# Optimization experiments

Hardware: AMD Instinct MI355X
Metric: run time of the kernel (lower is better)

The kernel has to match this reference:

```python
import jax, jax.numpy as jnp
import numpy as np

NUM_USERS = 1_000_000
NUM_ITEMS = 500_000
EMB = 64
H1, H2 = 256, 128
BATCH = 16384
BN_EPS = 1e-5


def setup_inputs() -> dict:
    key = jax.random.key(0)
    ks = jax.random.split(key, 16)
    inp = {
        "user_indices": jax.random.randint(ks[0], (BATCH,), 0, NUM_USERS),
        "item_indices": jax.random.randint(ks[1], (BATCH,), 0, NUM_ITEMS),
        # wide linear over concatenated one-hots == weight vector of len U+I
        "wide_w": jax.random.normal(ks[2], (NUM_USERS + NUM_ITEMS,), jnp.float32) * 0.01,
        "wide_b": jnp.zeros((1,), jnp.float32),
        "user_table": jax.random.normal(ks[3], (NUM_USERS, EMB), jnp.float32) * 0.05,
        "item_table": jax.random.normal(ks[4], (NUM_ITEMS, EMB), jnp.float32) * 0.05,
        "W1": jax.random.normal(ks[5], (H1, 2 * EMB), jnp.float32) * (1.0 / np.sqrt(2 * EMB)),
        "b1": jnp.zeros((H1,), jnp.float32),
        "g1": jnp.ones((H1,), jnp.float32),
        "be1": jnp.zeros((H1,), jnp.float32),
        "W2": jax.random.normal(ks[6], (H2, H1), jnp.float32) * (1.0 / np.sqrt(H1)),
        "b2": jnp.zeros((H2,), jnp.float32),
        "g2": jnp.ones((H2,), jnp.float32),
        "be2": jnp.zeros((H2,), jnp.float32),
        "W3": jax.random.normal(ks[7], (1, H2), jnp.float32) * (1.0 / np.sqrt(H2)),
        "b3": jnp.zeros((1,), jnp.float32),
    }
    return inp


def _block(x, W, b, g, be):
    # Linear -> ReLU -> BatchNorm1d (training-mode batch stats); Dropout is identity in eval.
    h = jnp.maximum(x @ W.T + b, 0.0)
    mu = jnp.mean(h, axis=0)
    var = jnp.mean((h - mu) ** 2, axis=0)  # biased var, as torch BN normalization
    return g * (h - mu) * jax.lax.rsqrt(var + BN_EPS) + be


def reference(user_indices, item_indices, wide_w, wide_b, user_table, item_table,
              W1, b1, g1, be1, W2, b2, g2, be2, W3, b3):
    # Wide path: one-hot scatter + Linear(.,1) == 2-row gather of wide_w + bias
    wide = wide_w[user_indices] + wide_w[item_indices + user_table.shape[0]] + wide_b[0]  # (B,)
    # Deep path
    x = jnp.concatenate([user_table[user_indices], item_table[item_indices]], axis=1)  # (B, 2E)
    h = _block(x, W1, b1, g1, be1)
    h = _block(h, W2, b2, g2, be2)
    deep = h @ W3.T + b3  # (B, 1)
    return jax.nn.sigmoid(wide[:, None] + deep)
```

## Files before the change

kernel.cpp:

```cpp
#include <hip/hip_runtime.h>
#include <math.h>

constexpr float INV_B = 1.0f / 16384.0f;
constexpr float BN_EPS_C = 1e-5f;
constexpr int NUM_USERS_C = 1000000;

typedef __attribute__((ext_vector_type(8))) short bf16x8;
typedef __attribute__((ext_vector_type(4))) float f32x4;

__device__ inline unsigned short f2bf(float f) {
    union { float f; unsigned u; } v; v.f = f;
    unsigned r = v.u + 0x7FFFu + ((v.u >> 16) & 1u);
    return (unsigned short)(r >> 16);
}
__device__ inline float bf2f(unsigned short h) {
    union { unsigned u; float f; } v; v.u = ((unsigned)h) << 16; return v.f;
}
__device__ inline bf16x8 pack8(float4 a, float4 b) {
    bf16x8 sv;
    sv[0] = (short)f2bf(a.x); sv[1] = (short)f2bf(a.y);
    sv[2] = (short)f2bf(a.z); sv[3] = (short)f2bf(a.w);
    sv[4] = (short)f2bf(b.x); sv[5] = (short)f2bf(b.y);
    sv[6] = (short)f2bf(b.z); sv[7] = (short)f2bf(b.w);
    return sv;
}
__device__ inline unsigned swz256(int r, int kb) { return (unsigned)(r * 256 + (kb ^ ((r & 7) << 4))); }
__device__ inline unsigned swz512(int r, int kb) { return (unsigned)(r * 512 + (kb ^ ((r & 7) << 4))); }

__global__ __launch_bounds__(256) void wd_k0(
    const float* __restrict__ W1, const float* __restrict__ W2,
    unsigned short* __restrict__ img1, unsigned short* __restrict__ img2,
    float* __restrict__ stats)
{
    int t = blockIdx.x * 256 + threadIdx.x;
    if (t < 12288) stats[t] = 0.f;
    if (t < 4096) {
        int a = t * 16, n = a >> 8, ks = a & 255;
        int k0 = (ks ^ ((n & 7) << 4)) >> 1;
        const float* src = W1 + (size_t)n * 128 + k0;
        float4 va = ((const float4*)src)[0];
        float4 vb = ((const float4*)src)[1];
        *(bf16x8*)((char*)img1 + a) = pack8(va, vb);
    } else if (t < 8192) {
        int tt = t - 4096;
        int a = tt * 16, h = a >> 15, rem = a & 32767, n = rem >> 8, ks = rem & 255;
        int kb = ks ^ ((n & 7) << 4);
        int k0 = h * 128 + (kb >> 1);
        const float* src = W2 + (size_t)n * 256 + k0;
        float4 va = ((const float4*)src)[0];
        float4 vb = ((const float4*)src)[1];
        *(bf16x8*)((char*)img2 + a) = pack8(va, vb);
    }
}

__global__ __launch_bounds__(512, 4) void wd_k1(
    const int* __restrict__ ui, const int* __restrict__ ii,
    const float* __restrict__ utab, const float* __restrict__ itab,
    const unsigned short* __restrict__ img1, const float* __restrict__ b1,
    unsigned short* __restrict__ h1s, float* __restrict__ part1)
{
    __shared__ char Xs[8192];
    __shared__ char Bnc[16384];
    __shared__ float sstat[512];

    const int tid = threadIdx.x, bid = blockIdx.x, row0 = bid * 32;
    const int w = tid >> 6, lane = tid & 63, lr = lane & 15, lk = lane >> 4;

    bf16x8 bfr[2][4];
#pragma unroll
    for (int nj = 0; nj < 2; ++nj) {
        int n = w * 32 + nj * 16 + lr;
        const char* bp = (const char*)img1 + n * 256;
        int sx = (n & 7) << 4;
#pragma unroll
        for (int kst = 0; kst < 4; ++kst)
            bfr[nj][kst] = *(const bf16x8*)(bp + ((kst * 64 + lk * 16) ^ sx));
    }

    {
        int row = tid >> 4, kc = tid & 15;
        const float* src = (kc < 8)
            ? utab + (size_t)ui[row0 + row] * 64 + kc * 8
            : itab + (size_t)ii[row0 + row] * 64 + (kc - 8) * 8;
        float4 a = ((const float4*)src)[0];
        float4 b = ((const float4*)src)[1];
        *(bf16x8*)(Xs + swz256(row, kc * 16)) = pack8(a, b);
    }
    __syncthreads();

    f32x4 acc[2][2];
#pragma unroll
    for (int mi = 0; mi < 2; ++mi)
#pragma unroll
        for (int nj = 0; nj < 2; ++nj) acc[mi][nj] = (f32x4){0.f, 0.f, 0.f, 0.f};

#pragma unroll
    for (int kst = 0; kst < 4; ++kst) {
        int kb = kst * 64 + lk * 16;
        bf16x8 a0 = *(const bf16x8*)(Xs + swz256(lr, kb));
        bf16x8 a1v = *(const bf16x8*)(Xs + swz256(16 + lr, kb));
#pragma unroll
        for (int nj = 0; nj < 2; ++nj) {
            acc[0][nj] = __builtin_amdgcn_mfma_f32_16x16x32_bf16(a0, bfr[nj][kst], acc[0][nj], 0, 0, 0);
            acc[1][nj] = __builtin_amdgcn_mfma_f32_16x16x32_bf16(a1v, bfr[nj][kst], acc[1][nj], 0, 0, 0);
        }
    }

#pragma unroll
    for (int nj = 0; nj < 2; ++nj) {
        int col = w * 32 + nj * 16 + lr;
        float bias = b1[col];
        float s = 0.f, q = 0.f;
#pragma unroll
        for (int mi = 0; mi < 2; ++mi)
#pragma unroll
            for (int reg = 0; reg < 4; ++reg) {
                int rl = mi * 16 + lk * 4 + reg;
                float v = fmaxf(acc[mi][nj][reg] + bias, 0.f);
                unsigned short hb = f2bf(v);
                float vr = bf2f(hb);
                s += vr; q += vr * vr;
                *(unsigned short*)(Bnc + swz512(rl, col * 2)) = hb;
            }
        s += __shfl_xor(s, 16); s += __shfl_xor(s, 32);
        q += __shfl_xor(q, 16); q += __shfl_xor(q, 32);
        if (lk == 0) { sstat[col] = s; sstat[256 + col] = q; }
    }
    __syncthreads();

    {
        const char* s0 = Bnc + tid * 32;
        char* d0 = (char*)h1s + (size_t)bid * 16384 + tid * 32;
        *(bf16x8*)d0 = *(const bf16x8*)s0;
        *(bf16x8*)(d0 + 16) = *(const bf16x8*)(s0 + 16);
    }
    atomicAdd(&part1[(size_t)(bid & 15) * 512 + tid], sstat[tid]);
}

__global__ __launch_bounds__(512, 4) void wd_k2(
    const unsigned short* __restrict__ h1s, const float* __restrict__ part1,
    const float* __restrict__ g1, const float* __restrict__ be1,
    const unsigned short* __restrict__ img2, const float* __restrict__ b2,
    unsigned short* __restrict__ h2s, float* __restrict__ part2)
{
    __shared__ char As[16384];
    __shared__ char Bnc[8192];
    __shared__ float a1s[256], c1s[256], sstat[256];

    const int tid = threadIdx.x, bid = blockIdx.x;
    const int w = tid >> 6, lane = tid & 63, lr = lane & 15, lk = lane >> 4;
    const int n = w * 16 + lr;
    const int sx = (n & 7) << 4;

    bf16x8 bfr[8];
#pragma unroll
    for (int h = 0; h < 2; ++h)
#pragma unroll
        for (int kst = 0; kst < 4; ++kst)
            bfr[h * 4 + kst] = *(const bf16x8*)((const char*)img2 + h * 32768 + n * 256 + ((kst * 64 + lk * 16) ^ sx));

    if (tid < 256) {
        float s = 0.f, q = 0.f;
#pragma unroll
        for (int r = 0; r < 16; ++r) { s += part1[r * 512 + tid]; q += part1[r * 512 + 256 + tid]; }
        float mu = s * INV_B;
        float var = fmaf(q, INV_B, -mu * mu);
        float rs = rsqrtf(var + BN_EPS_C);
        float a = g1[tid] * rs;
        a1s[tid] = a;
        c1s[tid] = fmaf(-mu, a, be1[tid]);
    }
    __syncthreads();

#pragma unroll
    for (int it = 0; it < 2; ++it) {
        int a = (it * 512 + tid) * 16;
        int r = a >> 9, ks = a & 511;
        int k0 = (ks ^ ((r & 7) << 4)) >> 1;
        bf16x8 hv = *(const bf16x8*)((const char*)h1s + (size_t)bid * 16384 + a);
        bf16x8 sv;
#pragma unroll
        for (int j = 0; j < 8; ++j) {
            float f = bf2f((unsigned short)hv[j]);
            f = fmaf(a1s[k0 + j], f, c1s[k0 + j]);
            sv[j] = (short)f2bf(f);
        }
        *(bf16x8*)(As + a) = sv;
    }
    __syncthreads();

    f32x4 acc[2];
    acc[0] = (f32x4){0.f, 0.f, 0.f, 0.f};
    acc[1] = (f32x4){0.f, 0.f, 0.f, 0.f};
#pragma unroll
    for (int k8 = 0; k8 < 8; ++k8) {
        int kb = (k8 * 64 + lk * 16) ^ ((lr & 7) << 4);
        bf16x8 a0 = *(const bf16x8*)(As + lr * 512 + kb);
        bf16x8 a1v = *(const bf16x8*)(As + (16 + lr) * 512 + kb);
        acc[0] = __builtin_amdgcn_mfma_f32_16x16x32_bf16(a0, bfr[k8], acc[0], 0, 0, 0);
        acc[1] = __builtin_amdgcn_mfma_f32_16x16x32_bf16(a1v, bfr[k8], acc[1], 0, 0, 0);
    }

    {
        float bias = b2[n];
        float s = 0.f, q = 0.f;
#pragma unroll
        for (int mi = 0; mi < 2; ++mi)
#pragma unroll
            for (int reg = 0; reg < 4; ++reg) {
                int rl = mi * 16 + lk * 4 + reg;
                float v = fmaxf(acc[mi][reg] + bias, 0.f);
                unsigned short hb = f2bf(v);
                float vr = bf2f(hb);
                s += vr; q += vr * vr;
                *(unsigned short*)(Bnc + swz256(rl, n * 2)) = hb;
            }
        s += __shfl_xor(s, 16); s += __shfl_xor(s, 32);
        q += __shfl_xor(q, 16); q += __shfl_xor(q, 32);
        if (lk == 0) { sstat[n] = s; sstat[128 + n] = q; }
    }
    __syncthreads();

    *(bf16x8*)((char*)h2s + (size_t)bid * 8192 + tid * 16) = *(const bf16x8*)(Bnc + tid * 16);
    if (tid < 256) atomicAdd(&part2[(size_t)(bid & 15) * 256 + tid], sstat[tid]);
}

__global__ __launch_bounds__(256, 2) void wd_k3(
    const int* __restrict__ ui, const int* __restrict__ ii,
    const float* __restrict__ wide_w, const float* __restrict__ wide_b,
    const unsigned short* __restrict__ h2s, const float* __restrict__ part2,
    const float* __restrict__ g2, const float* __restrict__ be2,
    const float* __restrict__ W3, const float* __restrict__ b3,
    float* __restrict__ out)
{
    __shared__ float af[128], cf[128];
    const int tid = threadIdx.x, bid = blockIdx.x;
    const int r = tid >> 2, kq = tid & 3;
    const int row = bid * 64 + r;

    float wide = 0.f;
    if (kq == 0) wide = wide_w[ui[row]] + wide_w[NUM_USERS_C + ii[row]];

    if (tid < 128) {
        float s = 0.f, q = 0.f;
#pragma unroll
        for (int rr = 0; rr < 16; ++rr) { s += part2[rr * 256 + tid]; q += part2[rr * 256 + 128 + tid]; }
        float mu = s * INV_B;
        float var = fmaf(q, INV_B, -mu * mu);
        float rs = rsqrtf(var + BN_EPS_C);
        float a = g2[tid] * rs;
        float c = fmaf(-mu, a, be2[tid]);
        float w3 = W3[tid];
        af[tid] = a * w3;
        cf[tid] = c * w3;
    }
    __syncthreads();

    const int tile = row >> 5, rin = row & 31;
    const char* tb = (const char*)h2s + (size_t)tile * 8192 + rin * 256;
    float acc = 0.f;
#pragma unroll
    for (int j = 0; j < 4; ++j) {
        int ks = (kq * 64 + j * 16) ^ ((rin & 7) << 4);
        bf16x8 hv = *(const bf16x8*)(tb + ks);
#pragma unroll
        for (int e = 0; e < 8; ++e) {
            float h = bf2f((unsigned short)hv[e]);
            int k = kq * 32 + j * 8 + e;
            acc += fmaf(h, af[k], cf[k]);
        }
    }
    acc += __shfl_xor(acc, 1);
    acc += __shfl_xor(acc, 2);
    if (kq == 0) {
        float logit = acc + b3[0] + wide_b[0] + wide;
        out[row] = 1.f / (1.f + expf(-logit));
    }
}

extern "C" void kernel_launch(void* const* d_in, const int* in_sizes, int n_in,
                              void* d_out, int out_size, void* d_ws, size_t ws_size,
                              hipStream_t stream)
{
    const int*   ui     = (const int*)d_in[0];
    const int*   ii     = (const int*)d_in[1];
    const float* wide_w = (const float*)d_in[2];
    const float* wide_b = (const float*)d_in[3];
    const float* utab   = (const float*)d_in[4];
    const float* itab   = (const float*)d_in[5];
    const float* W1     = (const float*)d_in[6];
    const float* b1     = (const float*)d_in[7];
    const float* g1     = (const float*)d_in[8];
    const float* be1    = (const float*)d_in[9];
    const float* W2     = (const float*)d_in[10];
    const float* b2     = (const float*)d_in[11];
    const float* g2     = (const float*)d_in[12];
    const float* be2    = (const float*)d_in[13];
    const float* W3     = (const float*)d_in[14];
    const float* b3     = (const float*)d_in[15];
    float* outp = (float*)d_out;

    char* base = (char*)d_ws;
    float* part1 = (float*)base;
    float* part2 = (float*)(base + 16 * 512 * 4);
    unsigned short* img1 = (unsigned short*)(base + 49152);
    unsigned short* img2 = (unsigned short*)(base + 49152 + 65536);
    unsigned short* h1s  = (unsigned short*)(base + 49152 + 131072);
    unsigned short* h2s  = (unsigned short*)(base + 49152 + 131072 + (size_t)512 * 16384);

    wd_k0<<<48, 256, 0, stream>>>(W1, W2, img1, img2, part1);
    wd_k1<<<512, 512, 0, stream>>>(ui, ii, utab, itab, img1, b1, h1s, part1);
    wd_k2<<<512, 512, 0, stream>>>(h1s, part1, g1, be1, img2, b2, h2s, part2);
    wd_k3<<<256, 256, 0, stream>>>(ui, ii, wide_w, wide_b, h2s, part2, g2, be2, W3, b3, outp);
}
```

Baseline: 28.99 us.

## Fuse all stages into one persistent kernel with grid barriers for BN stats

Replaces the four-kernel pipeline with a single 256-block kernel. Each block handles 64 rows end to end, keeping the hidden activations in shared memory, and uses global atomic counters as grid-wide barriers to wait for the batch-norm statistics. Weight repacking to bf16 now happens per block directly from fp32 in registers, removing the prep kernel. The layer-3 dot product is folded into the layer-2 epilogue through shuffles. This removes launch overhead and the global round trips for h1 and h2. The cost is redundant weight conversion in every block and a spin barrier that deadlocks unless all 256 blocks are co-resident.

After: 65.99 us. 128% more time.

```diff
diff --git a/kernel.cpp b/kernel.cpp
--- a/kernel.cpp
+++ b/kernel.cpp
@@ -4,6 +4,7 @@
 constexpr float INV_B = 1.0f / 16384.0f;
 constexpr float BN_EPS_C = 1e-5f;
 constexpr int NUM_USERS_C = 1000000;
+#define NBLK 256
 
 typedef __attribute__((ext_vector_type(8))) short bf16x8;
 typedef __attribute__((ext_vector_type(4))) float f32x4;
@@ -27,58 +28,51 @@
 __device__ inline unsigned swz256(int r, int kb) { return (unsigned)(r * 256 + (kb ^ ((r & 7) << 4))); }
 __device__ inline unsigned swz512(int r, int kb) { return (unsigned)(r * 512 + (kb ^ ((r & 7) << 4))); }
 
-__global__ __launch_bounds__(256) void wd_k0(
-    const float* __restrict__ W1, const float* __restrict__ W2,
-    unsigned short* __restrict__ img1, unsigned short* __restrict__ img2,
-    float* __restrict__ stats)
+__device__ inline void gbar(int* cnt) {
+    __syncthreads();
+    if (threadIdx.x == 0) {
+        __threadfence();
+        __hip_atomic_fetch_add(cnt, 1, __ATOMIC_ACQ_REL, __HIP_MEMORY_SCOPE_AGENT);
+        while (__hip_atomic_load(cnt, __ATOMIC_ACQUIRE, __HIP_MEMORY_SCOPE_AGENT) < NBLK)
+            __builtin_amdgcn_s_sleep(8);
+    }
+    __syncthreads();
+}
+
+__global__ __launch_bounds__(512, 2) void wd_fused(
+    const int* __restrict__ ui, const int* __restrict__ ii,
+    const float* __restrict__ wide_w, const float* __restrict__ wide_b,
+    const float* __restrict__ utab, const float* __restrict__ itab,
+    const float* __restrict__ W1, const float* __restrict__ b1,
+    const float* __restrict__ g1, const float* __restrict__ be1,
+    const float* __restrict__ W2, const float* __restrict__ b2,
+    const float* __restrict__ g2, const float* __restrict__ be2,
+    const float* __restrict__ W3, const float* __restrict__ b3,
+    float* __restrict__ part1, float* __restrict__ part2,
+    int* __restrict__ cnt1, int* __restrict__ cnt2,
+    float* __restrict__ out)
 {
-    int t = blockIdx.x * 256 + threadIdx.x;
-    if (t < 12288) stats[t] = 0.f;
-    if (t < 4096) {
-        int a = t * 16, n = a >> 8, ks = a & 255;
-        int k0 = (ks ^ ((n & 7) << 4)) >> 1;
-        const float* src = W1 + (size_t)n * 128 + k0;
-        float4 va = ((const float4*)src)[0];
-        float4 vb = ((const float4*)src)[1];
-        *(bf16x8*)((char*)img1 + a) = pack8(va, vb);
-    } else if (t < 8192) {
-        int tt = t - 4096;
-        int a = tt * 16, h = a >> 15, rem = a & 32767, n = rem >> 8, ks = rem & 255;
-        int kb = ks ^ ((n & 7) << 4);
-        int k0 = h * 128 + (kb >> 1);
-        const float* src = W2 + (size_t)n * 256 + k0;
-        float4 va = ((const float4*)src)[0];
-        float4 vb = ((const float4*)src)[1];
-        *(bf16x8*)((char*)img2 + a) = pack8(va, vb);
-    }
-}
-
-__global__ __launch_bounds__(512, 4) void wd_k1(
-    const int* __restrict__ ui, const int* __restrict__ ii,
-    const float* __restrict__ utab, const float* __restrict__ itab,
-    const unsigned short* __restrict__ img1, const float* __restrict__ b1,
-    unsigned short* __restrict__ h1s, float* __restrict__ part1)
-{
-    __shared__ char Xs[8192];
-    __shared__ char Bnc[16384];
+    __shared__ char Xs[16384];
+    __shared__ char Hs[32768];
     __shared__ float sstat[512];
-
-    const int tid = threadIdx.x, bid = blockIdx.x, row0 = bid * 32;
+    __shared__ float a1s[256], c1s[256];
+    __shared__ float af[128], cf[128];
+    __shared__ float red[512];
+    __shared__ float wide_s[64];
+    __shared__ float C2s;
+
+    const int tid = threadIdx.x, bid = blockIdx.x, row0 = bid * 64;
     const int w = tid >> 6, lane = tid & 63, lr = lane & 15, lk = lane >> 4;
-
-    bf16x8 bfr[2][4];
-#pragma unroll
-    for (int nj = 0; nj < 2; ++nj) {
-        int n = w * 32 + nj * 16 + lr;
-        const char* bp = (const char*)img1 + n * 256;
-        int sx = (n & 7) << 4;
-#pragma unroll
-        for (int kst = 0; kst < 4; ++kst)
-            bfr[nj][kst] = *(const bf16x8*)(bp + ((kst * 64 + lk * 16) ^ sx));
-    }
-
-    {
-        int row = tid >> 4, kc = tid & 15;
+    const int mh = w >> 2, nq = w & 3;
+
+    sstat[tid] = 0.f;
+
+    if (tid < 64)
+        wide_s[tid] = wide_w[ui[row0 + tid]] + wide_w[NUM_USERS_C + ii[row0 + tid]];
+
+#pragma unroll
+    for (int it = 0; it < 2; ++it) {
+        int idx = it * 512 + tid, row = idx >> 4, kc = idx & 15;
         const float* src = (kc < 8)
             ? utab + (size_t)ui[row0 + row] * 64 + kc * 8
             : itab + (size_t)ii[row0 + row] * 64 + (kc - 8) * 8;
@@ -86,83 +80,80 @@
         float4 b = ((const float4*)src)[1];
         *(bf16x8*)(Xs + swz256(row, kc * 16)) = pack8(a, b);
     }
-    __syncthreads();
-
-    f32x4 acc[2][2];
+
+    bf16x8 b1f[4][4];
+#pragma unroll
+    for (int nj = 0; nj < 4; ++nj) {
+        int n = nq * 64 + nj * 16 + lr;
+        const float* wp = W1 + (size_t)n * 128 + lk * 8;
+#pragma unroll
+        for (int kst = 0; kst < 4; ++kst) {
+            float4 va = ((const float4*)(wp + kst * 32))[0];
+            float4 vb = ((const float4*)(wp + kst * 32))[1];
+            b1f[nj][kst] = pack8(va, vb);
+        }
+    }
+    __syncthreads();
+
+    f32x4 acc1[2][4];
 #pragma unroll
     for (int mi = 0; mi < 2; ++mi)
 #pragma unroll
-        for (int nj = 0; nj < 2; ++nj) acc[mi][nj] = (f32x4){0.f, 0.f, 0.f, 0.f};
-
+        for (int nj = 0; nj < 4; ++nj) acc1[mi][nj] = (f32x4){0.f, 0.f, 0.f, 0.f};
 #pragma unroll
     for (int kst = 0; kst < 4; ++kst) {
         int kb = kst * 64 + lk * 16;
-        bf16x8 a0 = *(const bf16x8*)(Xs + swz256(lr, kb));
-        bf16x8 a1v = *(const bf16x8*)(Xs + swz256(16 + lr, kb));
-#pragma unroll
-        for (int nj = 0; nj < 2; ++nj) {
-            acc[0][nj] = __builtin_amdgcn_mfma_f32_16x16x32_bf16(a0, bfr[nj][kst], acc[0][nj], 0, 0, 0);
-            acc[1][nj] = __builtin_amdgcn_mfma_f32_16x16x32_bf16(a1v, bfr[nj][kst], acc[1][nj], 0, 0, 0);
-        }
-    }
-
-#pragma unroll
-    for (int nj = 0; nj < 2; ++nj) {
-        int col = w * 32 + nj * 16 + lr;
+        bf16x8 a0 = *(const bf16x8*)(Xs + swz256(mh * 32 + lr, kb));
+        bf16x8 a1 = *(const bf16x8*)(Xs + swz256(mh * 32 + 16 + lr, kb));
+#pragma unroll
+        for (int nj = 0; nj < 4; ++nj) {
+            acc1[0][nj] = __builtin_amdgcn_mfma_f32_16x16x32_bf16(a0, b1f[nj][kst], acc1[0][nj], 0, 0, 0);
+            acc1[1][nj] = __builtin_amdgcn_mfma_f32_16x16x32_bf16(a1, b1f[nj][kst], acc1[1][nj], 0, 0, 0);
+        }
+    }
+
+    const int n2 = w * 16 + lr;
+    bf16x8 b2f[8];
+#pragma unroll
+    for (int k8 = 0; k8 < 8; ++k8) {
+        const float* wp = W2 + (size_t)n2 * 256 + k8 * 32 + lk * 8;
+        float4 va = ((const float4*)wp)[0];
+        float4 vb = ((const float4*)wp)[1];
+        b2f[k8] = pack8(va, vb);
+    }
+
+#pragma unroll
+    for (int nj = 0; nj < 4; ++nj) {
+        int col = nq * 64 + nj * 16 + lr;
         float bias = b1[col];
         float s = 0.f, q = 0.f;
 #pragma unroll
         for (int mi = 0; mi < 2; ++mi)
 #pragma unroll
             for (int reg = 0; reg < 4; ++reg) {
-                int rl = mi * 16 + lk * 4 + reg;
-                float v = fmaxf(acc[mi][nj][reg] + bias, 0.f);
+                int rl = mh * 32 + mi * 16 + lk * 4 + reg;
+                float v = fmaxf(acc1[mi][nj][reg] + bias, 0.f);
                 unsigned short hb = f2bf(v);
                 float vr = bf2f(hb);
                 s += vr; q += vr * vr;
-                *(unsigned short*)(Bnc + swz512(rl, col * 2)) = hb;
+                *(unsigned short*)(Hs + swz512(rl, col * 2)) = hb;
             }
         s += __shfl_xor(s, 16); s += __shfl_xor(s, 32);
         q += __shfl_xor(q, 16); q += __shfl_xor(q, 32);
-        if (lk == 0) { sstat[col] = s; sstat[256 + col] = q; }
-    }
-    __syncthreads();
-
-    {
-        const char* s0 = Bnc + tid * 32;
-        char* d0 = (char*)h1s + (size_t)bid * 16384 + tid * 32;
-        *(bf16x8*)d0 = *(const bf16x8*)s0;
-        *(bf16x8*)(d0 + 16) = *(const bf16x8*)(s0 + 16);
-    }
-    atomicAdd(&part1[(size_t)(bid & 15) * 512 + tid], sstat[tid]);
-}
-
-__global__ __launch_bounds__(512, 4) void wd_k2(
-    const unsigned short* __restrict__ h1s, const float* __restrict__ part1,
-    const float* __restrict__ g1, const float* __restrict__ be1,
-    const unsigned short* __restrict__ img2, const float* __restrict__ b2,
-    unsigned short* __restrict__ h2s, float* __restrict__ part2)
-{
-    __shared__ char As[16384];
-    __shared__ char Bnc[8192];
-    __shared__ float a1s[256], c1s[256], sstat[256];
-
-    const int tid = threadIdx.x, bid = blockIdx.x;
-    const int w = tid >> 6, lane = tid & 63, lr = lane & 15, lk = lane >> 4;
-    const int n = w * 16 + lr;
-    const int sx = (n & 7) << 4;
-
-    bf16x8 bfr[8];
-#pragma unroll
-    for (int h = 0; h < 2; ++h)
-#pragma unroll
-        for (int kst = 0; kst < 4; ++kst)
-            bfr[h * 4 + kst] = *(const bf16x8*)((const char*)img2 + h * 32768 + n * 256 + ((kst * 64 + lk * 16) ^ sx));
+        if (lk == 0) { atomicAdd(&sstat[col], s); atomicAdd(&sstat[256 + col], q); }
+    }
+    __syncthreads();
+    atomicAdd(&part1[(size_t)(bid & 7) * 512 + tid], sstat[tid]);
+
+    gbar(cnt1);
 
     if (tid < 256) {
         float s = 0.f, q = 0.f;
 #pragma unroll
-        for (int r = 0; r < 16; ++r) { s += part1[r * 512 + tid]; q += part1[r * 512 + 256 + tid]; }
+        for (int r = 0; r < 8; ++r) {
+            s += __hip_atomic_load(&part1[r * 512 + tid], __ATOMIC_RELAXED, __HIP_MEMORY_SCOPE_AGENT);
+            q += __hip_atomic_load(&part1[r * 512 + 256 + tid], __ATOMIC_RELAXED, __HIP_MEMORY_SCOPE_AGENT);
+        }
         float mu = s * INV_B;
         float var = fmaf(q, INV_B, -mu * mu);
         float rs = rsqrtf(var + BN_EPS_C);
@@ -173,11 +164,10 @@
     __syncthreads();
 
 #pragma unroll
-    for (int it = 0; it < 2; ++it) {
-        int a = (it * 512 + tid) * 16;
-        int r = a >> 9, ks = a & 511;
+    for (int it = 0; it < 4; ++it) {
+        int a = (it * 512 + tid) * 16, r = a >> 9, ks = a & 511;
         int k0 = (ks ^ ((r & 7) << 4)) >> 1;
-        bf16x8 hv = *(const bf16x8*)((const char*)h1s + (size_t)bid * 16384 + a);
+        bf16x8 hv = *(bf16x8*)(Hs + a);
         bf16x8 sv;
 #pragma unroll
         for (int j = 0; j < 8; ++j) {
@@ -185,66 +175,52 @@
             f = fmaf(a1s[k0 + j], f, c1s[k0 + j]);
             sv[j] = (short)f2bf(f);
         }
-        *(bf16x8*)(As + a) = sv;
-    }
-    __syncthreads();
-
-    f32x4 acc[2];
-    acc[0] = (f32x4){0.f, 0.f, 0.f, 0.f};
-    acc[1] = (f32x4){0.f, 0.f, 0.f, 0.f};
+        *(bf16x8*)(Hs + a) = sv;
+    }
+    __syncthreads();
+
+    f32x4 acc2[4];
+#pragma unroll
+    for (int mi = 0; mi < 4; ++mi) acc2[mi] = (f32x4){0.f, 0.f, 0.f, 0.f};
+    const int sx2 = (lr & 7) << 4;
 #pragma unroll
     for (int k8 = 0; k8 < 8; ++k8) {
-        int kb = (k8 * 64 + lk * 16) ^ ((lr & 7) << 4);
-        bf16x8 a0 = *(const bf16x8*)(As + lr * 512 + kb);
-        bf16x8 a1v = *(const bf16x8*)(As + (16 + lr) * 512 + kb);
-        acc[0] = __builtin_amdgcn_mfma_f32_16x16x32_bf16(a0, bfr[k8], acc[0], 0, 0, 0);
-        acc[1] = __builtin_amdgcn_mfma_f32_16x16x32_bf16(a1v, bfr[k8], acc[1], 0, 0, 0);
+        int kb = (k8 * 64 + lk * 16) ^ sx2;
+#pragma unroll
+        for (int mi = 0; mi < 4; ++mi) {
+            bf16x8 a = *(const bf16x8*)(Hs + (mi * 16 + lr) * 512 + kb);
+            acc2[mi] = __builtin_amdgcn_mfma_f32_16x16x32_bf16(a, b2f[k8], acc2[mi], 0, 0, 0);
+        }
     }
 
     {
-        float bias = b2[n];
+        float bias = b2[n2];
         float s = 0.f, q = 0.f;
 #pragma unroll
-        for (int mi = 0; mi < 2; ++mi)
+        for (int mi = 0; mi < 4; ++mi)
 #pragma unroll
             for (int reg = 0; reg < 4; ++reg) {
-                int rl = mi * 16 + lk * 4 + reg;
-                float v = fmaxf(acc[mi][reg] + bias, 0.f);
-                unsigned short hb = f2bf(v);
-                float vr = bf2f(hb);
+                float v = fmaxf(acc2[mi][reg] + bias, 0.f);
+                float vr = bf2f(f2bf(v));
+                acc2[mi][reg] = vr;
                 s += vr; q += vr * vr;
-                *(unsigned short*)(Bnc + swz256(rl, n * 2)) = hb;
             }
         s += __shfl_xor(s, 16); s += __shfl_xor(s, 32);
         q += __shfl_xor(q, 16); q += __shfl_xor(q, 32);
-        if (lk == 0) { sstat[n] = s; sstat[128 + n] = q; }
-    }
-    __syncthreads();
-
-    *(bf16x8*)((char*)h2s + (size_t)bid * 8192 + tid * 16) = *(const bf16x8*)(Bnc + tid * 16);
-    if (tid < 256) atomicAdd(&part2[(size_t)(bid & 15) * 256 + tid], sstat[tid]);
-}
-
-__global__ __launch_bounds__(256, 2) void wd_k3(
-    const int* __restrict__ ui, const int* __restrict__ ii,
-    const float* __restrict__ wide_w, const float* __restrict__ wide_b,
-    const unsigned short* __restrict__ h2s, const float* __restrict__ part2,
-    const float* __restrict__ g2, const float* __restrict__ be2,
-    const float* __restrict__ W3, const float* __restrict__ b3,
-    float* __restrict__ out)
-{
-    __shared__ float af[128], cf[128];
-    const int tid = threadIdx.x, bid = blockIdx.x;
-    const int r = tid >> 2, kq = tid & 3;
-    const int row = bid * 64 + r;
-
-    float wide = 0.f;
-    if (kq == 0) wide = wide_w[ui[row]] + wide_w[NUM_USERS_C + ii[row]];
+        if (lk == 0) { sstat[n2] = s; sstat[128 + n2] = q; }
+    }
+    __syncthreads();
+    if (tid < 256) atomicAdd(&part2[(size_t)(bid & 7) * 256 + tid], sstat[tid]);
+
+    gbar(cnt2);
 
     if (tid < 128) {
         float s = 0.f, q = 0.f;
 #pragma unroll
-        for (int rr = 0; rr < 16; ++rr) { s += part2[rr * 256 + tid]; q += part2[rr * 256 + 128 + tid]; }
+        for (int r = 0; r < 8; ++r) {
+            s += __hip_atomic_load(&part2[r * 256 + tid], __ATOMIC_RELAXED, __HIP_MEMORY_SCOPE_AGENT);
+            q += __hip_atomic_load(&part2[r * 256 + 128 + tid], __ATOMIC_RELAXED, __HIP_MEMORY_SCOPE_AGENT);
+        }
         float mu = s * INV_B;
         float var = fmaf(q, INV_B, -mu * mu);
         float rs = rsqrtf(var + BN_EPS_C);
@@ -255,26 +231,37 @@
         cf[tid] = c * w3;
     }
     __syncthreads();
-
-    const int tile = row >> 5, rin = row & 31;
-    const char* tb = (const char*)h2s + (size_t)tile * 8192 + rin * 256;
-    float acc = 0.f;
-#pragma unroll
-    for (int j = 0; j < 4; ++j) {
-        int ks = (kq * 64 + j * 16) ^ ((rin & 7) << 4);
-        bf16x8 hv = *(const bf16x8*)(tb + ks);
-#pragma unroll
-        for (int e = 0; e < 8; ++e) {
-            float h = bf2f((unsigned short)hv[e]);
-            int k = kq * 32 + j * 8 + e;
-            acc += fmaf(h, af[k], cf[k]);
-        }
-    }
-    acc += __shfl_xor(acc, 1);
-    acc += __shfl_xor(acc, 2);
-    if (kq == 0) {
-        float logit = acc + b3[0] + wide_b[0] + wide;
-        out[row] = 1.f / (1.f + expf(-logit));
+    if (tid < 64) {
+        float x = cf[tid] + cf[tid + 64];
+        x += __shfl_xor(x, 1);  x += __shfl_xor(x, 2);  x += __shfl_xor(x, 4);
+        x += __shfl_xor(x, 8);  x += __shfl_xor(x, 16); x += __shfl_xor(x, 32);
+        if (tid == 0) C2s = x;
+    }
+
+    float pr[4][4];
+#pragma unroll
+    for (int mi = 0; mi < 4; ++mi)
+#pragma unroll
+        for (int reg = 0; reg < 4; ++reg) {
+            float t = af[n2] * acc2[mi][reg];
+            t += __shfl_xor(t, 1); t += __shfl_xor(t, 2);
+            t += __shfl_xor(t, 4); t += __shfl_xor(t, 8);
+            pr[mi][reg] = t;
+        }
+    if (lr == 0) {
+#pragma unroll
+        for (int mi = 0; mi < 4; ++mi)
+#pragma unroll
+            for (int reg = 0; reg < 4; ++reg)
+                red[w * 64 + mi * 16 + lk * 4 + reg] = pr[mi][reg];
+    }
+    __syncthreads();
+    if (tid < 64) {
+        float d = 0.f;
+#pragma unroll
+        for (int ww = 0; ww < 8; ++ww) d += red[ww * 64 + tid];
+        float logit = d + C2s + b3[0] + wide_b[0] + wide_s[tid];
+        out[row0 + tid] = 1.f / (1.f + expf(-logit));
     }
 }
 
@@ -302,14 +289,14 @@
 
     char* base = (char*)d_ws;
     float* part1 = (float*)base;
-    float* part2 = (float*)(base + 16 * 512 * 4);
-    unsigned short* img1 = (unsigned short*)(base + 49152);
-    unsigned short* img2 = (unsigned short*)(base + 49152 + 65536);
-    unsigned short* h1s  = (unsigned short*)(base + 49152 + 131072);
-    unsigned short* h2s  = (unsigned short*)(base + 49152 + 131072 + (size_t)512 * 16384);
-
-    wd_k0<<<48, 256, 0, stream>>>(W1, W2, img1, img2, part1);
-    wd_k1<<<512, 512, 0, stream>>>(ui, ii, utab, itab, img1, b1, h1s, part1);
-    wd_k2<<<512, 512, 0, stream>>>(h1s, part1, g1, be1, img2, b2, h2s, part2);
-    wd_k3<<<256, 256, 0, stream>>>(ui, ii, wide_w, wide_b, h2s, part2, g2, be2, W3, b3, outp);
-}
+    float* part2 = (float*)(base + 16384);
+    int*   cnt1  = (int*)(base + 16384 + 8192);
+    int*   cnt2  = cnt1 + 1;
+
+    hipMemsetAsync(base, 0, 16384 + 8192 + 8, stream);
+
+    wd_fused<<<NBLK, 512, 0, stream>>>(
+        ui, ii, wide_w, wide_b, utab, itab,
+        W1, b1, g1, be1, W2, b2, g2, be2, W3, b3,
+        part1, part2, cnt1, cnt2, outp);
+}
```

## Drop weight-prep kernel; convert weights to bf16 inline with packed cvt

Applied to the files above, without the earlier changes.

Removes the separate kernel that converted W1/W2 into swizzled bf16 images and zeroed the stats buffers. Each block of k1 and k2 now reads the fp32 weights directly and converts them in registers using the hardware v_cvt_pk_bf16_f32 instruction, and a hipMemsetAsync zeroes the stats instead. The intent is to save one kernel launch and the round trip through global memory for the images. In exchange every block reloads twice as many fp32 weight bytes, the memset is its own stream operation, and rounding now comes from the hardware conversion rather than the manual round-to-nearest-even code.

Measured after the change: 39.61 us. 1.37x slower.

```diff
diff --git a/kernel.cpp b/kernel.cpp
--- a/kernel.cpp
+++ b/kernel.cpp
@@ -16,47 +16,26 @@
 __device__ inline float bf2f(unsigned short h) {
     union { unsigned u; float f; } v; v.u = ((unsigned)h) << 16; return v.f;
 }
+__device__ inline unsigned cvt_pk(float lo, float hi) {
+    unsigned d;
+    asm("v_cvt_pk_bf16_f32 %0, %1, %2" : "=v"(d) : "v"(lo), "v"(hi));
+    return d;
+}
 __device__ inline bf16x8 pack8(float4 a, float4 b) {
-    bf16x8 sv;
-    sv[0] = (short)f2bf(a.x); sv[1] = (short)f2bf(a.y);
-    sv[2] = (short)f2bf(a.z); sv[3] = (short)f2bf(a.w);
-    sv[4] = (short)f2bf(b.x); sv[5] = (short)f2bf(b.y);
-    sv[6] = (short)f2bf(b.z); sv[7] = (short)f2bf(b.w);
-    return sv;
+    union { unsigned u[4]; bf16x8 v; } r;
+    r.u[0] = cvt_pk(a.x, a.y);
+    r.u[1] = cvt_pk(a.z, a.w);
+    r.u[2] = cvt_pk(b.x, b.y);
+    r.u[3] = cvt_pk(b.z, b.w);
+    return r.v;
 }
 __device__ inline unsigned swz256(int r, int kb) { return (unsigned)(r * 256 + (kb ^ ((r & 7) << 4))); }
 __device__ inline unsigned swz512(int r, int kb) { return (unsigned)(r * 512 + (kb ^ ((r & 7) << 4))); }
-
-__global__ __launch_bounds__(256) void wd_k0(
-    const float* __restrict__ W1, const float* __restrict__ W2,
-    unsigned short* __restrict__ img1, unsigned short* __restrict__ img2,
-    float* __restrict__ stats)
-{
-    int t = blockIdx.x * 256 + threadIdx.x;
-    if (t < 12288) stats[t] = 0.f;
-    if (t < 4096) {
-        int a = t * 16, n = a >> 8, ks = a & 255;
-        int k0 = (ks ^ ((n & 7) << 4)) >> 1;
-        const float* src = W1 + (size_t)n * 128 + k0;
-        float4 va = ((const float4*)src)[0];
-        float4 vb = ((const float4*)src)[1];
-        *(bf16x8*)((char*)img1 + a) = pack8(va, vb);
-    } else if (t < 8192) {
-        int tt = t - 4096;
-        int a = tt * 16, h = a >> 15, rem = a & 32767, n = rem >> 8, ks = rem & 255;
-        int kb = ks ^ ((n & 7) << 4);
-        int k0 = h * 128 + (kb >> 1);
-        const float* src = W2 + (size_t)n * 256 + k0;
-        float4 va = ((const float4*)src)[0];
-        float4 vb = ((const float4*)src)[1];
-        *(bf16x8*)((char*)img2 + a) = pack8(va, vb);
-    }
-}
 
 __global__ __launch_bounds__(512, 4) void wd_k1(
     const int* __restrict__ ui, const int* __restrict__ ii,
     const float* __restrict__ utab, const float* __restrict__ itab,
-    const unsigned short* __restrict__ img1, const float* __restrict__ b1,
+    const float* __restrict__ W1, const float* __restrict__ b1,
     unsigned short* __restrict__ h1s, float* __restrict__ part1)
 {
     __shared__ char Xs[8192];
@@ -70,11 +49,13 @@
 #pragma unroll
     for (int nj = 0; nj < 2; ++nj) {
         int n = w * 32 + nj * 16 + lr;
-        const char* bp = (const char*)img1 + n * 256;
-        int sx = (n & 7) << 4;
-#pragma unroll
-        for (int kst = 0; kst < 4; ++kst)
-            bfr[nj][kst] = *(const bf16x8*)(bp + ((kst * 64 + lk * 16) ^ sx));
+        const float* wp = W1 + (size_t)n * 128 + lk * 8;
+#pragma unroll
+        for (int kst = 0; kst < 4; ++kst) {
+            float4 va = ((const float4*)(wp + kst * 32))[0];
+            float4 vb = ((const float4*)(wp + kst * 32))[1];
+            bfr[nj][kst] = pack8(va, vb);
+        }
     }
 
     {
@@ -140,7 +121,7 @@
 __global__ __launch_bounds__(512, 4) void wd_k2(
     const unsigned short* __restrict__ h1s, const float* __restrict__ part1,
     const float* __restrict__ g1, const float* __restrict__ be1,
-    const unsigned short* __restrict__ img2, const float* __restrict__ b2,
+    const float* __restrict__ W2, const float* __restrict__ b2,
     unsigned short* __restrict__ h2s, float* __restrict__ part2)
 {
     __shared__ char As[16384];
@@ -150,14 +131,15 @@
     const int tid = threadIdx.x, bid = blockIdx.x;
     const int w = tid >> 6, lane = tid & 63, lr = lane & 15, lk = lane >> 4;
     const int n = w * 16 + lr;
-    const int sx = (n & 7) << 4;
 
     bf16x8 bfr[8];
 #pragma unroll
-    for (int h = 0; h < 2; ++h)
-#pragma unroll
-        for (int kst = 0; kst < 4; ++kst)
-            bfr[h * 4 + kst] = *(const bf16x8*)((const char*)img2 + h * 32768 + n * 256 + ((kst * 64 + lk * 16) ^ sx));
+    for (int k8 = 0; k8 < 8; ++k8) {
+        const float* wp = W2 + (size_t)n * 256 + k8 * 32 + lk * 8;
+        float4 va = ((const float4*)wp)[0];
+        float4 vb = ((const float4*)wp)[1];
+        bfr[k8] = pack8(va, vb);
+    }
 
     if (tid < 256) {
         float s = 0.f, q = 0.f;
@@ -180,10 +162,12 @@
         bf16x8 hv = *(const bf16x8*)((const char*)h1s + (size_t)bid * 16384 + a);
         bf16x8 sv;
 #pragma unroll
-        for (int j = 0; j < 8; ++j) {
-            float f = bf2f((unsigned short)hv[j]);
-            f = fmaf(a1s[k0 + j], f, c1s[k0 + j]);
-            sv[j] = (short)f2bf(f);
+        for (int j = 0; j < 8; j += 2) {
+            float f0 = fmaf(a1s[k0 + j],     bf2f((unsigned short)hv[j]),     c1s[k0 + j]);
+            float f1 = fmaf(a1s[k0 + j + 1], bf2f((unsigned short)hv[j + 1]), c1s[k0 + j + 1]);
+            unsigned pk = cvt_pk(f0, f1);
+            sv[j]     = (short)(pk & 0xFFFF);
+            sv[j + 1] = (short)(pk >> 16);
         }
         *(bf16x8*)(As + a) = sv;
     }
@@ -302,14 +286,13 @@
 
     char* base = (char*)d_ws;
     float* part1 = (float*)base;
-    float* part2 = (float*)(base + 16 * 512 * 4);
-    unsigned short* img1 = (unsigned short*)(base + 49152);
-    unsigned short* img2 = (unsigned short*)(base + 49152 + 65536);
-    unsigned short* h1s  = (unsigned short*)(base + 49152 + 131072);
-    unsigned short* h2s  = (unsigned short*)(base + 49152 + 131072 + (size_t)512 * 16384);
-
-    wd_k0<<<48, 256, 0, stream>>>(W1, W2, img1, img2, part1);
-    wd_k1<<<512, 512, 0, stream>>>(ui, ii, utab, itab, img1, b1, h1s, part1);
-    wd_k2<<<512, 512, 0, stream>>>(h1s, part1, g1, be1, img2, b2, h2s, part2);
+    float* part2 = (float*)(base + 32768);
+    unsigned short* h1s = (unsigned short*)(base + 49152);
+    unsigned short* h2s = (unsigned short*)(base + 49152 + (size_t)512 * 16384);
+
+    hipMemsetAsync(base, 0, 49152, stream);
+
+    wd_k1<<<512, 512, 0, stream>>>(ui, ii, utab, itab, W1, b1, h1s, part1);
+    wd_k2<<<512, 512, 0, stream>>>(h1s, part1, g1, be1, W2, b2, h2s, part2);
     wd_k3<<<256, 256, 0, stream>>>(ui, ii, wide_w, wide_b, h2s, part2, g2, be2, W3, b3, outp);
 }
```
